# Kernel optimization log

Hardware: AMD Instinct MI355X
Metric: run time of the kernel (lower is better)

Reference implementation:

```python
import jax, jax.numpy as jnp
import numpy as np

BLOCK_SIZE = 3
SOBEL_PAD = 1  # sobel_size // 2
BLOCK_PAD = BLOCK_SIZE // 2

_SOBEL_X = jnp.array([[-1.0, 0.0, 1.0], [-2.0, 0.0, 2.0], [-1.0, 0.0, 1.0]], dtype=jnp.float32)[None, None]
_SOBEL_Y = jnp.array([[-1.0, -2.0, -1.0], [0.0, 0.0, 0.0], [1.0, 2.0, 1.0]], dtype=jnp.float32)[None, None]
_SUM_K = jnp.ones((1, 1, BLOCK_SIZE, BLOCK_SIZE), dtype=jnp.float32)


def _pad_replicate(x, p):
    return jnp.pad(x, ((0, 0), (0, 0), (p, p), (p, p)), mode='edge')


def _conv(x, k):
    return jax.lax.conv_general_dilated(
        x, k, window_strides=(1, 1), padding='VALID',
        dimension_numbers=('NCHW', 'OIHW', 'NCHW'))


def setup_inputs() -> dict:
    key = jax.random.key(0)
    image = jax.random.uniform(key, (8, 1, 1080, 1920), dtype=jnp.float32) * 255.0
    return {"image": image}


def reference(image) -> jnp.ndarray:
    img = image.astype(jnp.float32)
    img_p = _pad_replicate(img, SOBEL_PAD)
    Ix = _conv(img_p, _SOBEL_X)
    Iy = _conv(img_p, _SOBEL_Y)
    Ixx = Ix * Ix
    Iyy = Iy * Iy
    Ixy = Ix * Iy
    sum_Ixx = _conv(_pad_replicate(Ixx, BLOCK_PAD), _SUM_K)
    sum_Iyy = _conv(_pad_replicate(Iyy, BLOCK_PAD), _SUM_K)
    sum_Ixy = _conv(_pad_replicate(Ixy, BLOCK_PAD), _SUM_K)
    half_trace = (sum_Ixx + sum_Iyy) * 0.5
    diff_half = (sum_Ixx - sum_Iyy) * 0.5
    sqrt_disc = jnp.sqrt(diff_half * diff_half + sum_Ixy * sum_Ixy + 1e-10)
    lambda_min = half_trace - sqrt_disc
    return jnp.clip(lambda_min, 0.0)
```

## Files before the change

kernel.cpp:

```cpp
#include <hip/hip_runtime.h>

typedef float v2f __attribute__((ext_vector_type(2)));
typedef float v4f __attribute__((ext_vector_type(4)));

#define IMG_H 1080
#define IMG_W 1920
#define NBATCH 8
#define LSTRIP 9
#define BROWS (4*LSTRIP)
#define NK (LSTRIP+4)
#define PF 4
#define RS 5


static __device__ __forceinline__ v2f vfma2(v2f a, v2f b, v2f c) {
    return __builtin_elementwise_fma(a, b, c);
}
static __device__ __forceinline__ float bperm(int addr, float v) {
    return __int_as_float(__builtin_amdgcn_ds_bpermute(addr, __float_as_int(v)));
}

__global__ __launch_bounds__(256, 3)
void shi_tomasi_kernel(const float* __restrict__ img, float* __restrict__ out) {
    const int cg    = threadIdx.x & 63;
    const int strip = threadIdx.x >> 6;
    const int bx    = blockIdx.x;
    const int base  = bx * 240;
    const int cl    = min(max(base - 8 + 4 * cg, 0), IMG_W - 4);
    const int c0    = base + 4 * (cg - 2);
    const int s0    = blockIdx.y * BROWS + strip * LSTRIP;
    const float* g  = img + (size_t)blockIdx.z * (IMG_H * IMG_W);
    float* outb     = out + (size_t)blockIdx.z * (IMG_H * IMG_W);

    const bool eL     = (bx == 0) && (cg == 2);
    const bool eR     = (bx == 7) && (cg == 61);
    const bool doSt   = (cg >= 2) && (cg < 62);
    const int  aLft   = 4 * (cg - 1);
    const int  aRgt   = 4 * (cg + 1);
    const bool topFix = (s0 == 0);
    const bool botFix = (s0 + LSTRIP == IMG_H);

    const float* lp = g + cl;

    v4f Zr[RS];
    #pragma unroll
    for (int k = 0; k < PF; ++k) {
        int lr = s0 - 2 + k;
        lr = max(0, min(IMG_H - 1, lr));
        Zr[k % RS] = *(const v4f*)(lp + (size_t)lr * IMG_W);
    }

    v2f hdR[3][3], hsR[3][3];
    float hfd[3], hfs[3];
    v2f hxx[3][2], hyy[3][2], hxy[3][2];
    const v2f two = {2.0f, 2.0f};

    #pragma unroll
    for (int k = 0; k < NK; ++k) {
        if (k + PF < NK) {
            int lr = s0 - 2 + k + PF;
            lr = max(0, min(IMG_H - 1, lr));
            Zr[(k + PF) % RS] = *(const v4f*)(lp + (size_t)lr * IMG_W);
        }

        {
            const v4f Z = Zr[k % RS];
            const float zl0 = bperm(aLft, Z.z), zl1 = bperm(aLft, Z.w);
            const float zr0 = bperm(aRgt, Z.x), zr1 = bperm(aRgt, Z.y);
            v2f Z0 = v2f{zl0, zl1};
            if (eL) Z0 = v2f{Z.x, Z.x};
            const v2f Z1 = v2f{Z.x, Z.y};
            const v2f Z2 = v2f{Z.z, Z.w};
            v2f Z3 = v2f{zr0, zr1};
            if (eR) Z3 = v2f{Z.w, Z.w};

            const v2f Sab = v2f{Z0.y, Z1.x};
            const v2f Sbc = v2f{Z1.y, Z2.x};
            const v2f Scd = v2f{Z2.y, Z3.x};
            v2f* hd = hdR[k % 3];
            v2f* hs = hsR[k % 3];
            hd[0] = Z1 - Z0; hd[1] = Z2 - Z1; hd[2] = Z3 - Z2;
            hs[0] = vfma2(Sab, two, Z0) + Z1;
            hs[1] = vfma2(Sbc, two, Z1) + Z2;
            hs[2] = vfma2(Scd, two, Z2) + Z3;
            hfd[k % 3] = eR ? (Z2.y - Z2.x) : (Z1.y - Z1.x);
            hfs[k % 3] = eR ? (Z2.x + 3.0f * Z2.y) : (3.0f * Z1.x + Z1.y);
        }

        if (k >= 2) {
            const int rr = k - 2;
            const int sm = rr % 3, sz = (rr + 1) % 3, sp = (rr + 2) % 3;

            v2f Ixp[3], Iyp[3];
            #pragma unroll
            for (int j = 0; j < 3; ++j) {
                Ixp[j] = vfma2(hdR[sz][j], two, hdR[sm][j]) + hdR[sp][j];
                Iyp[j] = hsR[sp][j] - hsR[sm][j];
            }
            const float ixf = hfd[sm] + 2.0f * hfd[sz] + hfd[sp];
            const float iyf = hfs[sp] - hfs[sm];
            if (eL) { Ixp[0].x = ixf; Iyp[0].x = iyf; }
            if (eR) { Ixp[2].y = ixf; Iyp[2].y = iyf; }

            v2f xx[3], yy[3], xy[3];
            #pragma unroll
            for (int j = 0; j < 3; ++j) {
                xx[j] = Ixp[j] * Ixp[j];
                yy[j] = Iyp[j] * Iyp[j];
                xy[j] = Ixp[j] * Iyp[j];
            }
            {
                v2f* hx = hxx[rr % 3];
                v2f* hy = hyy[rr % 3];
                v2f* hz = hxy[rr % 3];
                hx[0] = xx[0] + v2f{xx[0].y, xx[1].x} + xx[1];
                hx[1] = xx[1] + v2f{xx[1].y, xx[2].x} + xx[2];
                hy[0] = yy[0] + v2f{yy[0].y, yy[1].x} + yy[1];
                hy[1] = yy[1] + v2f{yy[1].y, yy[2].x} + yy[2];
                hz[0] = xy[0] + v2f{xy[0].y, xy[1].x} + xy[1];
                hz[1] = xy[1] + v2f{xy[1].y, xy[2].x} + xy[2];
            }
            if (rr == 1 && topFix) {
                #pragma unroll
                for (int q = 0; q < 2; ++q) {
                    hxx[0][q] = hxx[1][q]; hyy[0][q] = hyy[1][q]; hxy[0][q] = hxy[1][q];
                }
            }
            if (rr == LSTRIP + 1 && botFix) {
                #pragma unroll
                for (int q = 0; q < 2; ++q) {
                    hxx[rr % 3][q] = hxx[(rr - 1) % 3][q];
                    hyy[rr % 3][q] = hyy[(rr - 1) % 3][q];
                    hxy[rr % 3][q] = hxy[(rr - 1) % 3][q];
                }
            }

            if (rr >= 2) {
                const int a = (rr - 2) % 3, b2 = (rr - 1) % 3, c = rr % 3;
                float rv[4];
                #pragma unroll
                for (int q = 0; q < 2; ++q) {
                    const v2f sxx = hxx[a][q] + hxx[b2][q] + hxx[c][q];
                    const v2f syy = hyy[a][q] + hyy[b2][q] + hyy[c][q];
                    const v2f sxy = hxy[a][q] + hxy[b2][q] + hxy[c][q];
                    const v2f S = sxx + syy;
                    const v2f D = sxx - syy;
                    const v2f E = sxy + sxy;
                    const v2f disc = vfma2(D, D, vfma2(E, E, v2f{4e-10f, 4e-10f}));
                    const v2f qv = {__builtin_sqrtf(disc.x), __builtin_sqrtf(disc.y)};
                    const v2f lam = (S - qv) * 0.5f;
                    rv[2 * q]     = fmaxf(lam.x, 0.0f);
                    rv[2 * q + 1] = fmaxf(lam.y, 0.0f);
                }
                if (doSt) {
                    float* orowp = outb + (size_t)(s0 + rr - 2) * IMG_W + c0;
                    __builtin_nontemporal_store(v4f{rv[0], rv[1], rv[2], rv[3]},
                                                (v4f*)orowp);
                }
            }
        }
    }
}

extern "C" void kernel_launch(void* const* d_in, const int* in_sizes, int n_in,
                              void* d_out, int out_size, void* d_ws, size_t ws_size,
                              hipStream_t stream) {
    const float* img = (const float*)d_in[0];
    float* out = (float*)d_out;
    dim3 grid(8, IMG_H / BROWS, NBATCH);
    shi_tomasi_kernel<<<grid, 256, 0, stream>>>(img, out);
}
```

Before: 117.0 us.

## Process two batch images per thread to raise ILP and halve grid

Each thread now handles the same pixel strip in two images (batch z and z+4), interleaving their loads and compute. The aim is more memory-level parallelism and instruction-level parallelism per wave, with half as many blocks to launch. The cost is higher register pressure under launch_bounds(256,3), which could cause spills, and a smaller grid (960 blocks), which lowers occupancy and tail balance.

```diff
diff --git a/kernel.cpp b/kernel.cpp
--- a/kernel.cpp
+++ b/kernel.cpp
@@ -6,6 +6,7 @@
 #define IMG_H 1080
 #define IMG_W 1920
 #define NBATCH 8
+#define NI 2
 #define LSTRIP 9
 #define BROWS (4*LSTRIP)
 #define NK (LSTRIP+4)
@@ -29,8 +30,11 @@
     const int cl    = min(max(base - 8 + 4 * cg, 0), IMG_W - 4);
     const int c0    = base + 4 * (cg - 2);
     const int s0    = blockIdx.y * BROWS + strip * LSTRIP;
-    const float* g  = img + (size_t)blockIdx.z * (IMG_H * IMG_W);
-    float* outb     = out + (size_t)blockIdx.z * (IMG_H * IMG_W);
+    const size_t HW = (size_t)IMG_H * IMG_W;
+    const float* g0 = img + (size_t)blockIdx.z * HW;
+    const float* g1 = g0 + 4 * HW;
+    float* ob0      = out + (size_t)blockIdx.z * HW;
+    float* ob1      = ob0 + 4 * HW;
 
     const bool eL     = (bx == 0) && (cg == 2);
     const bool eR     = (bx == 7) && (cg == 61);
@@ -40,19 +44,21 @@
     const bool topFix = (s0 == 0);
     const bool botFix = (s0 + LSTRIP == IMG_H);
 
-    const float* lp = g + cl;
+    const float* lp0 = g0 + cl;
+    const float* lp1 = g1 + cl;
 
-    v4f Zr[RS];
+    v4f Zr[NI][RS];
     #pragma unroll
     for (int k = 0; k < PF; ++k) {
         int lr = s0 - 2 + k;
         lr = max(0, min(IMG_H - 1, lr));
-        Zr[k % RS] = *(const v4f*)(lp + (size_t)lr * IMG_W);
+        Zr[0][k % RS] = *(const v4f*)(lp0 + (size_t)lr * IMG_W);
+        Zr[1][k % RS] = *(const v4f*)(lp1 + (size_t)lr * IMG_W);
     }
 
-    v2f hdR[3][3], hsR[3][3];
-    float hfd[3], hfs[3];
-    v2f hxx[3][2], hyy[3][2], hxy[3][2];
+    v2f hdR[NI][3][3], hsR[NI][3][3];
+    float hfd[NI][3], hfs[NI][3];
+    v2f hxx[NI][3][2], hyy[NI][3][2], hxy[NI][3][2];
     const v2f two = {2.0f, 2.0f};
 
     #pragma unroll
@@ -60,11 +66,13 @@
         if (k + PF < NK) {
             int lr = s0 - 2 + k + PF;
             lr = max(0, min(IMG_H - 1, lr));
-            Zr[(k + PF) % RS] = *(const v4f*)(lp + (size_t)lr * IMG_W);
+            Zr[0][(k + PF) % RS] = *(const v4f*)(lp0 + (size_t)lr * IMG_W);
+            Zr[1][(k + PF) % RS] = *(const v4f*)(lp1 + (size_t)lr * IMG_W);
         }
 
-        {
-            const v4f Z = Zr[k % RS];
+        #pragma unroll
+        for (int im = 0; im < NI; ++im) {
+            const v4f Z = Zr[im][k % RS];
             const float zl0 = bperm(aLft, Z.z), zl1 = bperm(aLft, Z.w);
             const float zr0 = bperm(aRgt, Z.x), zr1 = bperm(aRgt, Z.y);
             v2f Z0 = v2f{zl0, zl1};
@@ -77,85 +85,91 @@
             const v2f Sab = v2f{Z0.y, Z1.x};
             const v2f Sbc = v2f{Z1.y, Z2.x};
             const v2f Scd = v2f{Z2.y, Z3.x};
-            v2f* hd = hdR[k % 3];
-            v2f* hs = hsR[k % 3];
+            v2f* hd = hdR[im][k % 3];
+            v2f* hs = hsR[im][k % 3];
             hd[0] = Z1 - Z0; hd[1] = Z2 - Z1; hd[2] = Z3 - Z2;
             hs[0] = vfma2(Sab, two, Z0) + Z1;
             hs[1] = vfma2(Sbc, two, Z1) + Z2;
             hs[2] = vfma2(Scd, two, Z2) + Z3;
-            hfd[k % 3] = eR ? (Z2.y - Z2.x) : (Z1.y - Z1.x);
-            hfs[k % 3] = eR ? (Z2.x + 3.0f * Z2.y) : (3.0f * Z1.x + Z1.y);
+            hfd[im][k % 3] = eR ? (Z2.y - Z2.x) : (Z1.y - Z1.x);
+            hfs[im][k % 3] = eR ? (Z2.x + 3.0f * Z2.y) : (3.0f * Z1.x + Z1.y);
         }
 
         if (k >= 2) {
             const int rr = k - 2;
             const int sm = rr % 3, sz = (rr + 1) % 3, sp = (rr + 2) % 3;
 
-            v2f Ixp[3], Iyp[3];
             #pragma unroll
-            for (int j = 0; j < 3; ++j) {
-                Ixp[j] = vfma2(hdR[sz][j], two, hdR[sm][j]) + hdR[sp][j];
-                Iyp[j] = hsR[sp][j] - hsR[sm][j];
-            }
-            const float ixf = hfd[sm] + 2.0f * hfd[sz] + hfd[sp];
-            const float iyf = hfs[sp] - hfs[sm];
-            if (eL) { Ixp[0].x = ixf; Iyp[0].x = iyf; }
-            if (eR) { Ixp[2].y = ixf; Iyp[2].y = iyf; }
+            for (int im = 0; im < NI; ++im) {
+                v2f Ixp[3], Iyp[3];
+                #pragma unroll
+                for (int j = 0; j < 3; ++j) {
+                    Ixp[j] = vfma2(hdR[im][sz][j], two, hdR[im][sm][j]) + hdR[im][sp][j];
+                    Iyp[j] = hsR[im][sp][j] - hsR[im][sm][j];
+                }
+                const float ixf = hfd[im][sm] + 2.0f * hfd[im][sz] + hfd[im][sp];
+                const float iyf = hfs[im][sp] - hfs[im][sm];
+                if (eL) { Ixp[0].x = ixf; Iyp[0].x = iyf; }
+                if (eR) { Ixp[2].y = ixf; Iyp[2].y = iyf; }
 
-            v2f xx[3], yy[3], xy[3];
-            #pragma unroll
-            for (int j = 0; j < 3; ++j) {
-                xx[j] = Ixp[j] * Ixp[j];
-                yy[j] = Iyp[j] * Iyp[j];
-                xy[j] = Ixp[j] * Iyp[j];
-            }
-            {
-                v2f* hx = hxx[rr % 3];
-                v2f* hy = hyy[rr % 3];
-                v2f* hz = hxy[rr % 3];
-                hx[0] = xx[0] + v2f{xx[0].y, xx[1].x} + xx[1];
-                hx[1] = xx[1] + v2f{xx[1].y, xx[2].x} + xx[2];
-                hy[0] = yy[0] + v2f{yy[0].y, yy[1].x} + yy[1];
-                hy[1] = yy[1] + v2f{yy[1].y, yy[2].x} + yy[2];
-                hz[0] = xy[0] + v2f{xy[0].y, xy[1].x} + xy[1];
-                hz[1] = xy[1] + v2f{xy[1].y, xy[2].x} + xy[2];
-            }
-            if (rr == 1 && topFix) {
+                v2f xx[3], yy[3], xy[3];
                 #pragma unroll
-                for (int q = 0; q < 2; ++q) {
-                    hxx[0][q] = hxx[1][q]; hyy[0][q] = hyy[1][q]; hxy[0][q] = hxy[1][q];
+                for (int j = 0; j < 3; ++j) {
+                    xx[j] = Ixp[j] * Ixp[j];
+                    yy[j] = Iyp[j] * Iyp[j];
+                    xy[j] = Ixp[j] * Iyp[j];
                 }
-            }
-            if (rr == LSTRIP + 1 && botFix) {
-                #pragma unroll
-                for (int q = 0; q < 2; ++q) {
-                    hxx[rr % 3][q] = hxx[(rr - 1) % 3][q];
-                    hyy[rr % 3][q] = hyy[(rr - 1) % 3][q];
-                    hxy[rr % 3][q] = hxy[(rr - 1) % 3][q];
+                {
+                    v2f* hx = hxx[im][rr % 3];
+                    v2f* hy = hyy[im][rr % 3];
+                    v2f* hz = hxy[im][rr % 3];
+                    hx[0] = xx[0] + v2f{xx[0].y, xx[1].x} + xx[1];
+                    hx[1] = xx[1] + v2f{xx[1].y, xx[2].x} + xx[2];
+                    hy[0] = yy[0] + v2f{yy[0].y, yy[1].x} + yy[1];
+                    hy[1] = yy[1] + v2f{yy[1].y, yy[2].x} + yy[2];
+                    hz[0] = xy[0] + v2f{xy[0].y, xy[1].x} + xy[1];
+                    hz[1] = xy[1] + v2f{xy[1].y, xy[2].x} + xy[2];
                 }
-            }
+                if (rr == 1 && topFix) {
+                    #pragma unroll
+                    for (int q = 0; q < 2; ++q) {
+                        hxx[im][0][q] = hxx[im][1][q];
+                        hyy[im][0][q] = hyy[im][1][q];
+                        hxy[im][0][q] = hxy[im][1][q];
+                    }
+                }
+                if (rr == LSTRIP + 1 && botFix) {
+                    #pragma unroll
+                    for (int q = 0; q < 2; ++q) {
+                        hxx[im][rr % 3][q] = hxx[im][(rr - 1) % 3][q];
+                        hyy[im][rr % 3][q] = hyy[im][(rr - 1) % 3][q];
+                        hxy[im][rr % 3][q] = hxy[im][(rr - 1) % 3][q];
+                    }
+                }
 
-            if (rr >= 2) {
-                const int a = (rr - 2) % 3, b2 = (rr - 1) % 3, c = rr % 3;
-                float rv[4];
-                #pragma unroll
-                for (int q = 0; q < 2; ++q) {
-                    const v2f sxx = hxx[a][q] + hxx[b2][q] + hxx[c][q];
-                    const v2f syy = hyy[a][q] + hyy[b2][q] + hyy[c][q];
-                    const v2f sxy = hxy[a][q] + hxy[b2][q] + hxy[c][q];
-                    const v2f S = sxx + syy;
-                    const v2f D = sxx - syy;
-                    const v2f E = sxy + sxy;
-                    const v2f disc = vfma2(D, D, vfma2(E, E, v2f{4e-10f, 4e-10f}));
-                    const v2f qv = {__builtin_sqrtf(disc.x), __builtin_sqrtf(disc.y)};
-                    const v2f lam = (S - qv) * 0.5f;
-                    rv[2 * q]     = fmaxf(lam.x, 0.0f);
-                    rv[2 * q + 1] = fmaxf(lam.y, 0.0f);
-                }
-                if (doSt) {
-                    float* orowp = outb + (size_t)(s0 + rr - 2) * IMG_W + c0;
-                    __builtin_nontemporal_store(v4f{rv[0], rv[1], rv[2], rv[3]},
-                                                (v4f*)orowp);
+                if (rr >= 2) {
+                    const int a = (rr - 2) % 3, b2 = (rr - 1) % 3, c = rr % 3;
+                    float rv[4];
+                    #pragma unroll
+                    for (int q = 0; q < 2; ++q) {
+                        const v2f sxx = hxx[im][a][q] + hxx[im][b2][q] + hxx[im][c][q];
+                        const v2f syy = hyy[im][a][q] + hyy[im][b2][q] + hyy[im][c][q];
+                        const v2f sxy = hxy[im][a][q] + hxy[im][b2][q] + hxy[im][c][q];
+                        const v2f S = sxx + syy;
+                        const v2f D = sxx - syy;
+                        const v2f E = sxy + sxy;
+                        const v2f disc = vfma2(D, D, vfma2(E, E, v2f{4e-10f, 4e-10f}));
+                        const v2f qv = {__builtin_sqrtf(disc.x), __builtin_sqrtf(disc.y)};
+                        const v2f lam = (S - qv) * 0.5f;
+                        rv[2 * q]     = fmaxf(lam.x, 0.0f);
+                        rv[2 * q + 1] = fmaxf(lam.y, 0.0f);
+                    }
+                    if (doSt) {
+                        float* orowp = (im == 0 ? ob0 : ob1)
+                                     + (size_t)(s0 + rr - 2) * IMG_W + c0;
+                        __builtin_nontemporal_store(v4f{rv[0], rv[1], rv[2], rv[3]},
+                                                    (v4f*)orowp);
+                    }
                 }
             }
         }
@@ -167,6 +181,6 @@
                               hipStream_t stream) {
     const float* img = (const float*)d_in[0];
     float* out = (float*)d_out;
-    dim3 grid(8, IMG_H / BROWS, NBATCH);
+    dim3 grid(8, IMG_H / BROWS, NBATCH / NI);
     shi_tomasi_kernel<<<grid, 256, 0, stream>>>(img, out);
 }
```

New measurement: 152.2 us. 1.3x slower.

## Replace cross-lane halo permutes with two overlapping vector loads per row

Applied to the files above, without the earlier changes.

Each thread now loads two overlapping 4-wide vectors per input row (offset -2 and +2 around its output columns) instead of one vector plus ds_bpermute exchanges with neighbour lanes. The packed v2f arithmetic becomes scalar float code over six columns, and the edge handling is simplified to copying the neighbouring gradient. Prefetch depth drops from 4 to 3 and launch bounds go from 3 to 2 blocks per CU. This removes the LDS permute traffic and its latency but doubles global load instructions (mostly cache hits) and may lose packed-math throughput.

```diff
diff --git a/kernel.cpp b/kernel.cpp
--- a/kernel.cpp
+++ b/kernel.cpp
@@ -1,6 +1,5 @@
 #include <hip/hip_runtime.h>
 
-typedef float v2f __attribute__((ext_vector_type(2)));
 typedef float v4f __attribute__((ext_vector_type(4)));
 
 #define IMG_H 1080
@@ -9,25 +8,19 @@
 #define LSTRIP 9
 #define BROWS (4*LSTRIP)
 #define NK (LSTRIP+4)
-#define PF 4
-#define RS 5
+#define PF 3
+#define RS 4
 
 
-static __device__ __forceinline__ v2f vfma2(v2f a, v2f b, v2f c) {
-    return __builtin_elementwise_fma(a, b, c);
-}
-static __device__ __forceinline__ float bperm(int addr, float v) {
-    return __int_as_float(__builtin_amdgcn_ds_bpermute(addr, __float_as_int(v)));
-}
-
-__global__ __launch_bounds__(256, 3)
+__global__ __launch_bounds__(256, 2)
 void shi_tomasi_kernel(const float* __restrict__ img, float* __restrict__ out) {
     const int cg    = threadIdx.x & 63;
     const int strip = threadIdx.x >> 6;
     const int bx    = blockIdx.x;
     const int base  = bx * 240;
-    const int cl    = min(max(base - 8 + 4 * cg, 0), IMG_W - 4);
     const int c0    = base + 4 * (cg - 2);
+    const int clA   = min(max(c0 - 2, 0), IMG_W - 4);
+    const int clB   = min(max(c0 + 2, 0), IMG_W - 4);
     const int s0    = blockIdx.y * BROWS + strip * LSTRIP;
     const float* g  = img + (size_t)blockIdx.z * (IMG_H * IMG_W);
     float* outb     = out + (size_t)blockIdx.z * (IMG_H * IMG_W);
@@ -35,122 +28,119 @@
     const bool eL     = (bx == 0) && (cg == 2);
     const bool eR     = (bx == 7) && (cg == 61);
     const bool doSt   = (cg >= 2) && (cg < 62);
-    const int  aLft   = 4 * (cg - 1);
-    const int  aRgt   = 4 * (cg + 1);
     const bool topFix = (s0 == 0);
     const bool botFix = (s0 + LSTRIP == IMG_H);
 
-    const float* lp = g + cl;
+    const float* lpA = g + clA;
+    const float* lpB = g + clB;
 
-    v4f Zr[RS];
+    v4f za[RS], zb[RS];
     #pragma unroll
     for (int k = 0; k < PF; ++k) {
-        int lr = s0 - 2 + k;
-        lr = max(0, min(IMG_H - 1, lr));
-        Zr[k % RS] = *(const v4f*)(lp + (size_t)lr * IMG_W);
+        int lr = max(0, min(IMG_H - 1, s0 - 2 + k));
+        za[k] = *(const v4f*)(lpA + (size_t)lr * IMG_W);
+        zb[k] = *(const v4f*)(lpB + (size_t)lr * IMG_W);
     }
 
-    v2f hdR[3][3], hsR[3][3];
-    float hfd[3], hfs[3];
-    v2f hxx[3][2], hyy[3][2], hxy[3][2];
-    const v2f two = {2.0f, 2.0f};
+    float cdR[3][6], hsR[3][6];
+    float hxx[3][4], hyy[3][4], hxy[3][4];
 
     #pragma unroll
     for (int k = 0; k < NK; ++k) {
         if (k + PF < NK) {
-            int lr = s0 - 2 + k + PF;
-            lr = max(0, min(IMG_H - 1, lr));
-            Zr[(k + PF) % RS] = *(const v4f*)(lp + (size_t)lr * IMG_W);
+            int lr = min(IMG_H - 1, s0 + k + (PF - 2));
+            za[(k + PF) % RS] = *(const v4f*)(lpA + (size_t)lr * IMG_W);
+            zb[(k + PF) % RS] = *(const v4f*)(lpB + (size_t)lr * IMG_W);
         }
 
         {
-            const v4f Z = Zr[k % RS];
-            const float zl0 = bperm(aLft, Z.z), zl1 = bperm(aLft, Z.w);
-            const float zr0 = bperm(aRgt, Z.x), zr1 = bperm(aRgt, Z.y);
-            v2f Z0 = v2f{zl0, zl1};
-            if (eL) Z0 = v2f{Z.x, Z.x};
-            const v2f Z1 = v2f{Z.x, Z.y};
-            const v2f Z2 = v2f{Z.z, Z.w};
-            v2f Z3 = v2f{zr0, zr1};
-            if (eR) Z3 = v2f{Z.w, Z.w};
+            const v4f A = za[k % RS];
+            const v4f B = zb[k % RS];
+            const float zm2 = A.x;
+            const float zm1 = eL ? A.x : A.y;
+            const float z0  = eL ? A.x : A.z;
+            const float z1  = eL ? A.y : A.w;
+            const float z2  = eR ? B.z : B.x;
+            const float z3  = eR ? B.w : B.y;
+            const float z4  = eR ? B.w : B.z;
+            const float z5  = B.w;
 
-            const v2f Sab = v2f{Z0.y, Z1.x};
-            const v2f Sbc = v2f{Z1.y, Z2.x};
-            const v2f Scd = v2f{Z2.y, Z3.x};
-            v2f* hd = hdR[k % 3];
-            v2f* hs = hsR[k % 3];
-            hd[0] = Z1 - Z0; hd[1] = Z2 - Z1; hd[2] = Z3 - Z2;
-            hs[0] = vfma2(Sab, two, Z0) + Z1;
-            hs[1] = vfma2(Sbc, two, Z1) + Z2;
-            hs[2] = vfma2(Scd, two, Z2) + Z3;
-            hfd[k % 3] = eR ? (Z2.y - Z2.x) : (Z1.y - Z1.x);
-            hfs[k % 3] = eR ? (Z2.x + 3.0f * Z2.y) : (3.0f * Z1.x + Z1.y);
+            float* cdw = cdR[k % 3];
+            float* hsw = hsR[k % 3];
+            cdw[0] = z0 - zm2;
+            cdw[1] = z1 - zm1;
+            cdw[2] = z2 - z0;
+            cdw[3] = z3 - z1;
+            cdw[4] = z4 - z2;
+            cdw[5] = z5 - z3;
+            hsw[0] = fmaf(2.0f, zm1, zm2) + z0;
+            hsw[1] = fmaf(2.0f, z0, zm1) + z1;
+            hsw[2] = fmaf(2.0f, z1, z0) + z2;
+            hsw[3] = fmaf(2.0f, z2, z1) + z3;
+            hsw[4] = fmaf(2.0f, z3, z2) + z4;
+            hsw[5] = fmaf(2.0f, z4, z3) + z5;
         }
 
         if (k >= 2) {
             const int rr = k - 2;
             const int sm = rr % 3, sz = (rr + 1) % 3, sp = (rr + 2) % 3;
 
-            v2f Ixp[3], Iyp[3];
+            float Ix[6], Iy[6];
             #pragma unroll
-            for (int j = 0; j < 3; ++j) {
-                Ixp[j] = vfma2(hdR[sz][j], two, hdR[sm][j]) + hdR[sp][j];
-                Iyp[j] = hsR[sp][j] - hsR[sm][j];
+            for (int p = 0; p < 6; ++p) {
+                Ix[p] = fmaf(2.0f, cdR[sz][p], cdR[sm][p]) + cdR[sp][p];
+                Iy[p] = hsR[sp][p] - hsR[sm][p];
             }
-            const float ixf = hfd[sm] + 2.0f * hfd[sz] + hfd[sp];
-            const float iyf = hfs[sp] - hfs[sm];
-            if (eL) { Ixp[0].x = ixf; Iyp[0].x = iyf; }
-            if (eR) { Ixp[2].y = ixf; Iyp[2].y = iyf; }
+            if (eL) { Ix[0] = Ix[1]; Iy[0] = Iy[1]; }
+            if (eR) { Ix[5] = Ix[4]; Iy[5] = Iy[4]; }
 
-            v2f xx[3], yy[3], xy[3];
+            float xx[6], yy[6], xy[6];
             #pragma unroll
-            for (int j = 0; j < 3; ++j) {
-                xx[j] = Ixp[j] * Ixp[j];
-                yy[j] = Iyp[j] * Iyp[j];
-                xy[j] = Ixp[j] * Iyp[j];
+            for (int p = 0; p < 6; ++p) {
+                xx[p] = Ix[p] * Ix[p];
+                yy[p] = Iy[p] * Iy[p];
+                xy[p] = Ix[p] * Iy[p];
             }
             {
-                v2f* hx = hxx[rr % 3];
-                v2f* hy = hyy[rr % 3];
-                v2f* hz = hxy[rr % 3];
-                hx[0] = xx[0] + v2f{xx[0].y, xx[1].x} + xx[1];
-                hx[1] = xx[1] + v2f{xx[1].y, xx[2].x} + xx[2];
-                hy[0] = yy[0] + v2f{yy[0].y, yy[1].x} + yy[1];
-                hy[1] = yy[1] + v2f{yy[1].y, yy[2].x} + yy[2];
-                hz[0] = xy[0] + v2f{xy[0].y, xy[1].x} + xy[1];
-                hz[1] = xy[1] + v2f{xy[1].y, xy[2].x} + xy[2];
+                float* hx = hxx[rr % 3];
+                float* hy = hyy[rr % 3];
+                float* hz = hxy[rr % 3];
+                #pragma unroll
+                for (int c = 0; c < 4; ++c) {
+                    hx[c] = (xx[c] + xx[c + 1]) + xx[c + 2];
+                    hy[c] = (yy[c] + yy[c + 1]) + yy[c + 2];
+                    hz[c] = (xy[c] + xy[c + 1]) + xy[c + 2];
+                }
             }
             if (rr == 1 && topFix) {
                 #pragma unroll
-                for (int q = 0; q < 2; ++q) {
-                    hxx[0][q] = hxx[1][q]; hyy[0][q] = hyy[1][q]; hxy[0][q] = hxy[1][q];
+                for (int c = 0; c < 4; ++c) {
+                    hxx[0][c] = hxx[1][c]; hyy[0][c] = hyy[1][c]; hxy[0][c] = hxy[1][c];
                 }
             }
             if (rr == LSTRIP + 1 && botFix) {
                 #pragma unroll
-                for (int q = 0; q < 2; ++q) {
-                    hxx[rr % 3][q] = hxx[(rr - 1) % 3][q];
-                    hyy[rr % 3][q] = hyy[(rr - 1) % 3][q];
-                    hxy[rr % 3][q] = hxy[(rr - 1) % 3][q];
+                for (int c = 0; c < 4; ++c) {
+                    hxx[rr % 3][c] = hxx[(rr - 1) % 3][c];
+                    hyy[rr % 3][c] = hyy[(rr - 1) % 3][c];
+                    hxy[rr % 3][c] = hxy[(rr - 1) % 3][c];
                 }
             }
 
             if (rr >= 2) {
-                const int a = (rr - 2) % 3, b2 = (rr - 1) % 3, c = rr % 3;
+                const int a = (rr - 2) % 3, b2 = (rr - 1) % 3, cc = rr % 3;
                 float rv[4];
                 #pragma unroll
-                for (int q = 0; q < 2; ++q) {
-                    const v2f sxx = hxx[a][q] + hxx[b2][q] + hxx[c][q];
-                    const v2f syy = hyy[a][q] + hyy[b2][q] + hyy[c][q];
-                    const v2f sxy = hxy[a][q] + hxy[b2][q] + hxy[c][q];
-                    const v2f S = sxx + syy;
-                    const v2f D = sxx - syy;
-                    const v2f E = sxy + sxy;
-                    const v2f disc = vfma2(D, D, vfma2(E, E, v2f{4e-10f, 4e-10f}));
-                    const v2f qv = {__builtin_sqrtf(disc.x), __builtin_sqrtf(disc.y)};
-                    const v2f lam = (S - qv) * 0.5f;
-                    rv[2 * q]     = fmaxf(lam.x, 0.0f);
-                    rv[2 * q + 1] = fmaxf(lam.y, 0.0f);
+                for (int c = 0; c < 4; ++c) {
+                    const float sxx = (hxx[a][c] + hxx[b2][c]) + hxx[cc][c];
+                    const float syy = (hyy[a][c] + hyy[b2][c]) + hyy[cc][c];
+                    const float sxy = (hxy[a][c] + hxy[b2][c]) + hxy[cc][c];
+                    const float S = sxx + syy;
+                    const float D = sxx - syy;
+                    const float E = sxy + sxy;
+                    const float disc = fmaf(D, D, fmaf(E, E, 4e-10f));
+                    const float q = __builtin_sqrtf(disc);
+                    rv[c] = fmaxf((S - q) * 0.5f, 0.0f);
                 }
                 if (doSt) {
                     float* orowp = outb + (size_t)(s0 + rr - 2) * IMG_W + c0;
```

Result: no change. 117.3 us (+0.2%).
